# Optimization experiments

Hardware: AMD Instinct MI355X
Metric: run time of the kernel (lower is better)

The kernel has to match this reference:

```python
import math
import jax, jax.numpy as jnp
import numpy as np

NUM_EXPERTS = 64
TOP_K = 2
CAPACITY_FACTOR = 1.25
B, D = 16384, 2048
H = D // 2


def setup_inputs() -> dict:
    key = jax.random.key(0)
    k0, k1, k2 = jax.random.split(key, 3)
    x = jax.random.normal(k0, (B, D), dtype=jnp.float32)
    W1 = jax.random.normal(k1, (D, H), dtype=jnp.float32) * 0.02
    b1 = jnp.zeros((H,), dtype=jnp.float32)
    W2 = jax.random.normal(k2, (H, NUM_EXPERTS), dtype=jnp.float32) * 0.02
    b2 = jnp.zeros((NUM_EXPERTS,), dtype=jnp.float32)
    return {"x": x, "W1": W1, "b1": b1, "W2": W2, "b2": b2}


def reference(x, W1, b1, W2, b2):
    # gate MLP: Linear -> SiLU -> Linear (eval mode: no routing noise)
    h = jax.nn.silu(x @ W1 + b1)            # [B, H]
    logits = h @ W2 + b2                    # [B, E]

    top_vals, top_idx = jax.lax.top_k(logits, TOP_K)   # [B, K]
    weights = jax.nn.softmax(top_vals, axis=-1)        # [B, K]

    # Switch-style load balance loss: E * sum_i f_i * P_i
    probs = jax.nn.softmax(logits, axis=-1)            # [B, E]
    top1 = jnp.argmax(logits, axis=-1)                 # [B] (non-diff)
    freq = jax.ops.segment_sum(jnp.ones((B,), dtype=logits.dtype), top1,
                               num_segments=NUM_EXPERTS) / B
    aux_loss = NUM_EXPERTS * jnp.sum(freq * probs.mean(axis=0))

    # Capacity-based drop. The torch loop iterates k-major, batch-minor and only
    # increments the counter on accepted tokens; since the counter saturates at
    # `capacity`, a token is dropped iff its rank among all prior occurrences of
    # the same expert (in k-major order) is >= capacity.
    capacity = max(1, math.ceil(B * TOP_K / NUM_EXPERTS * CAPACITY_FACTOR))
    idx_flat = top_idx.T.reshape(-1)                               # [K*B], k-major order
    onehot = (idx_flat[:, None] == jnp.arange(NUM_EXPERTS)).astype(jnp.int32)  # [K*B, E]
    excl_cumsum = jnp.cumsum(onehot, axis=0) - onehot              # prior count per expert
    ranks = jnp.take_along_axis(excl_cumsum, idx_flat[:, None], axis=1)[:, 0]  # [K*B]
    dropped_mask = (ranks >= capacity).reshape(TOP_K, B).T          # [B, K] bool

    return weights, top_idx, aux_loss, dropped_mask
```

## Files before the change

### kernel.cpp

```cpp
#include <hip/hip_runtime.h>
#include <stdint.h>

#define B_TOK   16384
#define D_IN    2048
#define H_DIM   1024
#define NEXP    64
#define CAPACITY 640

typedef __attribute__((ext_vector_type(8))) _Float16 half8;
typedef __attribute__((ext_vector_type(4))) float f32x4;

__device__ __forceinline__ void split16(float a, unsigned short& uh, unsigned short& ul) {
  union { _Float16 h; unsigned short u; } c;
  _Float16 h1 = (fabsf(a) < 1.220703125e-4f) ? (_Float16)0.0f : (_Float16)a;
  c.h = h1; uh = c.u;
  float r = (a - (float)h1) * 4096.0f;
  c.h = (_Float16)r; ul = c.u;
}

__device__ __forceinline__ void gload_lds16(const void* g, void* l) {
  __builtin_amdgcn_global_load_lds(
      (const __attribute__((address_space(1))) void*)g,
      (__attribute__((address_space(3))) void*)l, 16, 0, 0);
}

__global__ __launch_bounds__(256) void k_convA(const float* __restrict__ x,
                                               unsigned short* __restrict__ A2) {
  int tid = blockIdx.x * 256 + threadIdx.x;
  int f0 = tid * 4;
  int t = f0 >> 11;
  int k = f0 & 2047;
  float4 v = *reinterpret_cast<const float4*>(x + f0);
  ushort4 hi, lo;
  split16(v.x, hi.x, lo.x);
  split16(v.y, hi.y, lo.y);
  split16(v.z, hi.z, lo.z);
  split16(v.w, hi.w, lo.w);
  unsigned short* row = A2 + (size_t)t * 4096;
  *reinterpret_cast<ushort4*>(row + k)        = hi;
  *reinterpret_cast<ushort4*>(row + 2048 + k) = lo;
}

__global__ __launch_bounds__(256) void k_convB(const float* __restrict__ W1,
                                               unsigned short* __restrict__ B2t) {
  __shared__ float tile[32][33];
  int k0 = blockIdx.x * 32;
  int n0 = blockIdx.y * 32;
  int tx = threadIdx.x;
  int ty = threadIdx.y;
  #pragma unroll
  for (int i = 0; i < 32; i += 8)
    tile[ty + i][tx] = W1[(size_t)(k0 + ty + i) * 1024 + n0 + tx];
  __syncthreads();
  #pragma unroll
  for (int i = 0; i < 32; i += 8) {
    int n = n0 + ty + i;
    int k = k0 + tx;
    unsigned short uh, ul;
    split16(tile[tx][ty + i], uh, ul);
    unsigned short* row = B2t + (size_t)n * 4096;
    row[k]        = uh;
    row[2048 + k] = ul;
  }
}

__global__ __launch_bounds__(256) void k_gemm1(const unsigned short* __restrict__ A2,
                                               const unsigned short* __restrict__ B2t,
                                               const float* __restrict__ b1,
                                               float* __restrict__ h) {
  __shared__ unsigned short Al[128 * 64];
  __shared__ unsigned short Bl[128 * 64];
  int bid = blockIdx.x;
  int wg  = ((bid & 7) << 7) | (bid >> 3);
  int bm  = wg >> 3;
  int bn  = wg & 7;
  int row0 = bm << 7;
  int col0 = bn << 7;
  int tid  = threadIdx.x;
  int w    = tid >> 6;
  int lane = tid & 63;
  int wr = (w >> 1) << 6;
  int wc = (w & 1) << 6;

  int rsub = lane >> 3;
  int csub = (((lane & 7) ^ ((lane >> 3) & 7)) << 3);

  f32x4 acc[4][4] = {};

  int arow = wr + (lane & 15);
  int brow = wc + (lane & 15);
  int r7   = lane & 7;
  int cbase = lane >> 4;

  auto do_region = [&](int aoff, int boff) {
    for (int kt = 0; kt < 32; ++kt) {
      int kk0 = kt * 64;
      #pragma unroll
      for (int j = 0; j < 4; ++j) {
        int rs = (w * 4 + j) * 8;
        const unsigned short* ga = A2 + (size_t)(row0 + rs + rsub) * 4096 + aoff + kk0 + csub;
        gload_lds16(ga, (char*)Al + (w * 4 + j) * 1024);
        const unsigned short* gb = B2t + (size_t)(col0 + rs + rsub) * 4096 + boff + kk0 + csub;
        gload_lds16(gb, (char*)Bl + (w * 4 + j) * 1024);
      }
      __syncthreads();
      #pragma unroll
      for (int kk = 0; kk < 2; ++kk) {
        int cofs = ((kk * 4 + cbase) ^ r7) << 3;
        half8 af[4], bfr[4];
        #pragma unroll
        for (int m = 0; m < 4; ++m)
          af[m] = *reinterpret_cast<const half8*>(Al + (arow + m * 16) * 64 + cofs);
        #pragma unroll
        for (int n = 0; n < 4; ++n)
          bfr[n] = *reinterpret_cast<const half8*>(Bl + (brow + n * 16) * 64 + cofs);
        #pragma unroll
        for (int m = 0; m < 4; ++m)
          #pragma unroll
          for (int n = 0; n < 4; ++n)
            acc[m][n] = __builtin_amdgcn_mfma_f32_16x16x32_f16(af[m], bfr[n], acc[m][n], 0, 0, 0);
      }
      __syncthreads();
    }
  };

  auto scale_acc = [&](float s) {
    #pragma unroll
    for (int m = 0; m < 4; ++m)
      #pragma unroll
      for (int n = 0; n < 4; ++n)
        acc[m][n] *= s;
  };

  do_region(2048, 2048);
  scale_acc(2.44140625e-4f);
  do_region(0, 2048);
  do_region(2048, 0);
  scale_acc(2.44140625e-4f);
  do_region(0, 0);

  int crow0 = row0 + wr + ((lane >> 4) << 2);
  int ccol0 = col0 + wc + (lane & 15);
  #pragma unroll
  for (int n = 0; n < 4; ++n) {
    int col = ccol0 + n * 16;
    float bias = b1[col];
    #pragma unroll
    for (int m = 0; m < 4; ++m) {
      #pragma unroll
      for (int j = 0; j < 4; ++j) {
        int row = crow0 + m * 16 + j;
        float v = acc[m][n][j] + bias;
        float s = v / (1.0f + expf(-v));
        h[(size_t)row * 1024 + col] = s;
      }
    }
  }
}

__global__ __launch_bounds__(256) void k_gemm2p(const float* __restrict__ h,
                                                const float* __restrict__ W2,
                                                double* __restrict__ part) {
  __shared__ float ht[32][76];
  __shared__ float wt[32][64];
  int t0 = blockIdx.x * 64;
  int kbase = blockIdx.y * 256;
  int tid = threadIdx.x;
  int ig = tid & 15;
  int jg = tid >> 4;
  double acc[4][4] = {};

  for (int kc = 0; kc < 8; ++kc) {
    __syncthreads();
    #pragma unroll
    for (int q = 0; q < 8; ++q) {
      int f = tid + q * 256;
      int k = f & 31, t = f >> 5;
      ht[k][t] = h[(size_t)(t0 + t) * 1024 + kbase + kc * 32 + k];
    }
    #pragma unroll
    for (int q = 0; q < 8; ++q) {
      int f = tid + q * 256;
      int k = f >> 6, e = f & 63;
      wt[k][e] = W2[(size_t)(kbase + kc * 32 + k) * 64 + e];
    }
    __syncthreads();
    #pragma unroll
    for (int k = 0; k < 32; ++k) {
      float4 hv = *reinterpret_cast<const float4*>(&ht[k][ig * 4]);
      float4 wv = *reinterpret_cast<const float4*>(&wt[k][jg * 4]);
      double ha[4] = {(double)hv.x, (double)hv.y, (double)hv.z, (double)hv.w};
      double wa[4] = {(double)wv.x, (double)wv.y, (double)wv.z, (double)wv.w};
      #pragma unroll
      for (int a = 0; a < 4; ++a)
        #pragma unroll
        for (int b = 0; b < 4; ++b)
          acc[a][b] += ha[a] * wa[b];
    }
  }
  double* seg = part + (size_t)blockIdx.y * (B_TOK * NEXP);
  #pragma unroll
  for (int a = 0; a < 4; ++a) {
    int t = t0 + ig * 4 + a;
    #pragma unroll
    for (int b = 0; b < 4; ++b)
      seg[(size_t)t * 64 + jg * 4 + b] = acc[a][b];
  }
}

__global__ __launch_bounds__(256) void k_router(const double* __restrict__ part,
                                                const float* __restrict__ b2,
                                                float* __restrict__ out_w,
                                                float* __restrict__ out_idx,
                                                int* __restrict__ idx_ws,
                                                float* __restrict__ cnt,
                                                float* __restrict__ probsum) {
  int tid = threadIdx.x;
  int lane = tid & 63;
  int wv = tid >> 6;
  int gw = blockIdx.x * 4 + wv;
  const size_t seg = (size_t)B_TOK * NEXP;
  float accp = 0.f, accc = 0.f;
  for (int it = 0; it < 16; ++it) {
    int t = gw * 16 + it;
    size_t o = (size_t)t * 64 + lane;
    double sum = part[o] + part[o + seg] + part[o + 2 * seg] + part[o + 3 * seg]
               + (double)b2[lane];
    float v = (float)sum;
    float bv = v; int bi = lane;
    #pragma unroll
    for (int off = 32; off; off >>= 1) {
      float v2 = __shfl_xor(bv, off);
      int i2 = __shfl_xor(bi, off);
      if (v2 > bv || (v2 == bv && i2 < bi)) { bv = v2; bi = i2; }
    }
    float ve = (lane == bi) ? -3.4e38f : v;
    float bv2 = ve; int bi2 = lane;
    #pragma unroll
    for (int off = 32; off; off >>= 1) {
      float v2 = __shfl_xor(bv2, off);
      int i2 = __shfl_xor(bi2, off);
      if (v2 > bv2 || (v2 == bv2 && i2 < bi2)) { bv2 = v2; bi2 = i2; }
    }
    float p = expf(v - bv);
    float s = p;
    #pragma unroll
    for (int off = 32; off; off >>= 1) s += __shfl_xor(s, off);
    accp += p / s;
    accc += (lane == bi) ? 1.f : 0.f;
    if (lane == 0) {
      float e21 = expf(bv2 - bv);
      float w0 = 1.f / (1.f + e21);
      out_w[t * 2]     = w0;
      out_w[t * 2 + 1] = e21 / (1.f + e21);
      out_idx[t * 2]     = (float)bi;
      out_idx[t * 2 + 1] = (float)bi2;
      idx_ws[t * 2]     = bi;
      idx_ws[t * 2 + 1] = bi2;
    }
  }
  atomicAdd(&probsum[lane], accp);
  atomicAdd(&cnt[lane], accc);
}

__global__ void k_mask(const int* __restrict__ idx_ws, float* __restrict__ out_mask) {
  const int e = blockIdx.x;
  const int lane = threadIdx.x;
  const unsigned long long lt = (1ull << lane) - 1ull;
  int c = 0;
  for (int k = 0; k < 2; ++k) {
    for (int base = 0; base < B_TOK; base += 256) {
      int i0 = idx_ws[(base +       lane) * 2 + k];
      int i1 = idx_ws[(base + 64  + lane) * 2 + k];
      int i2 = idx_ws[(base + 128 + lane) * 2 + k];
      int i3 = idx_ws[(base + 192 + lane) * 2 + k];
      unsigned long long m0 = __ballot(i0 == e);
      unsigned long long m1 = __ballot(i1 == e);
      unsigned long long m2 = __ballot(i2 == e);
      unsigned long long m3 = __ballot(i3 == e);
      if (i0 == e) out_mask[(base +       lane) * 2 + k] = (c + __popcll(m0 & lt) >= CAPACITY) ? 1.f : 0.f;
      c += __popcll(m0);
      if (i1 == e) out_mask[(base + 64  + lane) * 2 + k] = (c + __popcll(m1 & lt) >= CAPACITY) ? 1.f : 0.f;
      c += __popcll(m1);
      if (i2 == e) out_mask[(base + 128 + lane) * 2 + k] = (c + __popcll(m2 & lt) >= CAPACITY) ? 1.f : 0.f;
      c += __popcll(m2);
      if (i3 == e) out_mask[(base + 192 + lane) * 2 + k] = (c + __popcll(m3 & lt) >= CAPACITY) ? 1.f : 0.f;
      c += __popcll(m3);
    }
  }
}

__global__ void k_aux(const float* __restrict__ cnt, const float* __restrict__ probsum,
                      float* __restrict__ out_aux) {
  int lane = threadIdx.x;
  float v = (cnt[lane] * (1.f / 16384.f)) * (probsum[lane] * (1.f / 16384.f));
  #pragma unroll
  for (int off = 32; off; off >>= 1) v += __shfl_xor(v, off);
  if (lane == 0) out_aux[0] = v * 64.f;
}

extern "C" void kernel_launch(void* const* d_in, const int* in_sizes, int n_in,
                              void* d_out, int out_size, void* d_ws, size_t ws_size,
                              hipStream_t stream) {
  const float* x  = (const float*)d_in[0];
  const float* W1 = (const float*)d_in[1];
  const float* b1 = (const float*)d_in[2];
  const float* W2 = (const float*)d_in[3];
  const float* b2 = (const float*)d_in[4];

  char* ws = (char*)d_ws;
  unsigned short* A2  = (unsigned short*)ws;
  unsigned short* B2t = (unsigned short*)(ws + 134217728);
  float* h            = (float*)(ws + 142606336);
  double* part  = (double*)ws;
  int*   idx_ws = (int*)(ws + 33554432);
  float* cnt     = (float*)(ws + 33554432 + 131072);
  float* probsum = (float*)(ws + 33554432 + 131072 + 256);

  float* out      = (float*)d_out;
  float* out_w    = out;
  float* out_idx  = out + 32768;
  float* out_aux  = out + 65536;
  float* out_mask = out + 65537;

  hipLaunchKernelGGL(k_convA, dim3(32768), dim3(256), 0, stream, x, A2);
  hipLaunchKernelGGL(k_convB, dim3(64, 32), dim3(32, 8), 0, stream, W1, B2t);
  hipLaunchKernelGGL(k_gemm1, dim3(1024), dim3(256), 0, stream, A2, B2t, b1, h);
  hipLaunchKernelGGL(k_gemm2p, dim3(256, 4), dim3(256), 0, stream, h, W2, part);
  hipMemsetAsync(ws + 33554432 + 131072, 0, 512, stream);
  hipLaunchKernelGGL(k_router, dim3(256), dim3(256), 0, stream,
                     part, b2, out_w, out_idx, idx_ws, cnt, probsum);
  hipLaunchKernelGGL(k_mask, dim3(64), dim3(64), 0, stream, idx_ws, out_mask);
  hipLaunchKernelGGL(k_aux, dim3(1), dim3(64), 0, stream, cnt, probsum, out_aux);
}
```

Baseline: 672.8 us.

## Run second gate GEMM on MFMA with split-fp16 operands instead of FP64

Replaces the FP64 FMA-based h@W2 kernel with an MFMA f16 kernel that uses a three-product hi/lo split (hi*hi plus a scaled hi*lo and lo*hi correction) for near-fp32 accuracy. gemm1 now writes h directly as split fp16 halves, and a new kernel pre-splits and transposes W2. The K split drops from 4 to 2, with fp32 partials instead of doubles, which cuts partial-sum traffic. The FP64 path is slow on this hardware, and this removes it. The risk is lower logit precision, which could flip top-k ties or capacity ranks.

Result: no change. 664.9 us (-1.2%).

```diff
diff --git a/kernel.cpp b/kernel.cpp
--- a/kernel.cpp
+++ b/kernel.cpp
@@ -64,10 +64,34 @@
   }
 }
 
+__global__ __launch_bounds__(256) void k_convW2(const float* __restrict__ W2,
+                                                unsigned short* __restrict__ W2t) {
+  __shared__ float tile[32][33];
+  int k0 = blockIdx.x * 32;
+  int e0 = blockIdx.y * 32;
+  int tx = threadIdx.x;
+  int ty = threadIdx.y;
+  #pragma unroll
+  for (int i = 0; i < 32; i += 8)
+    tile[ty + i][tx] = W2[(size_t)(k0 + ty + i) * 64 + e0 + tx];
+  __syncthreads();
+  #pragma unroll
+  for (int i = 0; i < 32; i += 8) {
+    int e = e0 + ty + i;
+    int k = k0 + tx;
+    unsigned short uh, ul;
+    split16(tile[tx][ty + i], uh, ul);
+    unsigned short* row = W2t + (size_t)e * 2048;
+    row[k]        = uh;
+    row[1024 + k] = ul;
+  }
+}
+
 __global__ __launch_bounds__(256) void k_gemm1(const unsigned short* __restrict__ A2,
                                                const unsigned short* __restrict__ B2t,
                                                const float* __restrict__ b1,
-                                               float* __restrict__ h) {
+                                               unsigned short* __restrict__ Hh,
+                                               unsigned short* __restrict__ Hm) {
   __shared__ unsigned short Al[128 * 64];
   __shared__ unsigned short Bl[128 * 64];
   int bid = blockIdx.x;
@@ -152,63 +176,83 @@
         int row = crow0 + m * 16 + j;
         float v = acc[m][n][j] + bias;
         float s = v / (1.0f + expf(-v));
-        h[(size_t)row * 1024 + col] = s;
+        unsigned short uh, ul;
+        split16(s, uh, ul);
+        Hh[(size_t)row * 1024 + col] = uh;
+        Hm[(size_t)row * 1024 + col] = ul;
       }
     }
   }
 }
 
-__global__ __launch_bounds__(256) void k_gemm2p(const float* __restrict__ h,
-                                                const float* __restrict__ W2,
-                                                double* __restrict__ part) {
-  __shared__ float ht[32][76];
-  __shared__ float wt[32][64];
+__global__ __launch_bounds__(256) void k_gemm2m(const unsigned short* __restrict__ Hh,
+                                                const unsigned short* __restrict__ Hm,
+                                                const unsigned short* __restrict__ W2t,
+                                                float* __restrict__ part) {
+  __shared__ unsigned short Ah[64 * 64];
+  __shared__ unsigned short Am[64 * 64];
+  __shared__ unsigned short Bh[64 * 64];
+  __shared__ unsigned short Bm[64 * 64];
   int t0 = blockIdx.x * 64;
-  int kbase = blockIdx.y * 256;
+  int kbase = blockIdx.y * 512;
   int tid = threadIdx.x;
-  int ig = tid & 15;
-  int jg = tid >> 4;
-  double acc[4][4] = {};
-
-  for (int kc = 0; kc < 8; ++kc) {
+  int w = tid >> 6;
+  int lane = tid & 63;
+  int rsub = lane >> 3;
+  int csub = (((lane & 7) ^ ((lane >> 3) & 7)) << 3);
+  int r7 = lane & 7;
+  int cbase = lane >> 4;
+  int arow = (w << 4) + (lane & 15);
+
+  f32x4 acc_h[4] = {};
+  f32x4 acc_c[4] = {};
+
+  for (int kt = 0; kt < 8; ++kt) {
+    int kk0 = kbase + kt * 64;
+    #pragma unroll
+    for (int j = 0; j < 2; ++j) {
+      int g = w * 2 + j;
+      int grow = g * 8 + rsub;
+      const unsigned short* gah = Hh + (size_t)(t0 + grow) * 1024 + kk0 + csub;
+      gload_lds16(gah, (char*)Ah + g * 1024);
+      const unsigned short* gam = Hm + (size_t)(t0 + grow) * 1024 + kk0 + csub;
+      gload_lds16(gam, (char*)Am + g * 1024);
+      const unsigned short* gbh = W2t + (size_t)grow * 2048 + kk0 + csub;
+      gload_lds16(gbh, (char*)Bh + g * 1024);
+      const unsigned short* gbm = W2t + (size_t)grow * 2048 + 1024 + kk0 + csub;
+      gload_lds16(gbm, (char*)Bm + g * 1024);
+    }
     __syncthreads();
     #pragma unroll
-    for (int q = 0; q < 8; ++q) {
-      int f = tid + q * 256;
-      int k = f & 31, t = f >> 5;
-      ht[k][t] = h[(size_t)(t0 + t) * 1024 + kbase + kc * 32 + k];
-    }
-    #pragma unroll
-    for (int q = 0; q < 8; ++q) {
-      int f = tid + q * 256;
-      int k = f >> 6, e = f & 63;
-      wt[k][e] = W2[(size_t)(kbase + kc * 32 + k) * 64 + e];
+    for (int kk = 0; kk < 2; ++kk) {
+      int cofs = ((kk * 4 + cbase) ^ r7) << 3;
+      half8 a_h = *reinterpret_cast<const half8*>(Ah + arow * 64 + cofs);
+      half8 a_m = *reinterpret_cast<const half8*>(Am + arow * 64 + cofs);
+      #pragma unroll
+      for (int n = 0; n < 4; ++n) {
+        int brow = n * 16 + (lane & 15);
+        half8 b_h = *reinterpret_cast<const half8*>(Bh + brow * 64 + cofs);
+        half8 b_m = *reinterpret_cast<const half8*>(Bm + brow * 64 + cofs);
+        acc_h[n] = __builtin_amdgcn_mfma_f32_16x16x32_f16(a_h, b_h, acc_h[n], 0, 0, 0);
+        acc_c[n] = __builtin_amdgcn_mfma_f32_16x16x32_f16(a_h, b_m, acc_c[n], 0, 0, 0);
+        acc_c[n] = __builtin_amdgcn_mfma_f32_16x16x32_f16(a_m, b_h, acc_c[n], 0, 0, 0);
+      }
     }
     __syncthreads();
-    #pragma unroll
-    for (int k = 0; k < 32; ++k) {
-      float4 hv = *reinterpret_cast<const float4*>(&ht[k][ig * 4]);
-      float4 wv = *reinterpret_cast<const float4*>(&wt[k][jg * 4]);
-      double ha[4] = {(double)hv.x, (double)hv.y, (double)hv.z, (double)hv.w};
-      double wa[4] = {(double)wv.x, (double)wv.y, (double)wv.z, (double)wv.w};
-      #pragma unroll
-      for (int a = 0; a < 4; ++a)
-        #pragma unroll
-        for (int b = 0; b < 4; ++b)
-          acc[a][b] += ha[a] * wa[b];
-    }
-  }
-  double* seg = part + (size_t)blockIdx.y * (B_TOK * NEXP);
-  #pragma unroll
-  for (int a = 0; a < 4; ++a) {
-    int t = t0 + ig * 4 + a;
-    #pragma unroll
-    for (int b = 0; b < 4; ++b)
-      seg[(size_t)t * 64 + jg * 4 + b] = acc[a][b];
-  }
-}
-
-__global__ __launch_bounds__(256) void k_router(const double* __restrict__ part,
+  }
+
+  float* seg = part + (size_t)blockIdx.y * (B_TOK * NEXP);
+  int trow0 = t0 + (w << 4) + ((lane >> 4) << 2);
+  int ecol0 = lane & 15;
+  #pragma unroll
+  for (int n = 0; n < 4; ++n)
+    #pragma unroll
+    for (int j = 0; j < 4; ++j)
+      seg[(size_t)(trow0 + j) * 64 + n * 16 + ecol0] =
+          acc_c[n][j] * 2.44140625e-4f + acc_h[n][j];
+}
+
+__global__ __launch_bounds__(256) void k_router(const float* __restrict__ part,
                                                 const float* __restrict__ b2,
                                                 float* __restrict__ out_w,
                                                 float* __restrict__ out_idx,
@@ -224,9 +268,7 @@
   for (int it = 0; it < 16; ++it) {
     int t = gw * 16 + it;
     size_t o = (size_t)t * 64 + lane;
-    double sum = part[o] + part[o + seg] + part[o + 2 * seg] + part[o + 3 * seg]
-               + (double)b2[lane];
-    float v = (float)sum;
+    float v = part[o] + part[o + seg] + b2[lane];
     float bv = v; int bi = lane;
     #pragma unroll
     for (int off = 32; off; off >>= 1) {
@@ -311,11 +353,13 @@
   char* ws = (char*)d_ws;
   unsigned short* A2  = (unsigned short*)ws;
   unsigned short* B2t = (unsigned short*)(ws + 134217728);
-  float* h            = (float*)(ws + 142606336);
-  double* part  = (double*)ws;
-  int*   idx_ws = (int*)(ws + 33554432);
-  float* cnt     = (float*)(ws + 33554432 + 131072);
-  float* probsum = (float*)(ws + 33554432 + 131072 + 256);
+  unsigned short* Hh  = (unsigned short*)(ws + 142606336);
+  unsigned short* Hm  = (unsigned short*)(ws + 176160768);
+  unsigned short* W2t = (unsigned short*)(ws + 209715200);
+  float* part    = (float*)ws;
+  int*   idx_ws  = (int*)(ws + 8388608);
+  float* cnt     = (float*)(ws + 8388608 + 131072);
+  float* probsum = (float*)(ws + 8388608 + 131072 + 256);
 
   float* out      = (float*)d_out;
   float* out_w    = out;
@@ -325,9 +369,10 @@
 
   hipLaunchKernelGGL(k_convA, dim3(32768), dim3(256), 0, stream, x, A2);
   hipLaunchKernelGGL(k_convB, dim3(64, 32), dim3(32, 8), 0, stream, W1, B2t);
-  hipLaunchKernelGGL(k_gemm1, dim3(1024), dim3(256), 0, stream, A2, B2t, b1, h);
-  hipLaunchKernelGGL(k_gemm2p, dim3(256, 4), dim3(256), 0, stream, h, W2, part);
-  hipMemsetAsync(ws + 33554432 + 131072, 0, 512, stream);
+  hipLaunchKernelGGL(k_convW2, dim3(32, 2), dim3(32, 8), 0, stream, W2, W2t);
+  hipLaunchKernelGGL(k_gemm1, dim3(1024), dim3(256), 0, stream, A2, B2t, b1, Hh, Hm);
+  hipLaunchKernelGGL(k_gemm2m, dim3(256, 2), dim3(256), 0, stream, Hh, Hm, W2t, part);
+  hipMemsetAsync(ws + 8388608 + 131072, 0, 512, stream);
   hipLaunchKernelGGL(k_router, dim3(256), dim3(256), 0, stream,
                      part, b2, out_w, out_idx, idx_ws, cnt, probsum);
   hipLaunchKernelGGL(k_mask, dim3(64), dim3(64), 0, stream, idx_ws, out_mask);
```
